# Optimization experiments

Hardware: AMD Instinct MI355X
Metric: run time of the kernel (lower is better)

The kernel has to match this reference:

```python
import jax, jax.numpy as jnp
from jax import lax
import numpy as np

B, H, W, D_MODEL = 2, 64, 64, 192
D_INNER, D_STATE, DT_RANK = 384, 16, 12
L = H * W
LN_EPS = 1e-5


def setup_inputs() -> dict:
    ks = jax.random.split(jax.random.key(0), 12)
    rng = np.random.default_rng(0)
    perm = rng.permutation(L).astype(np.int32)

    def p(i, shape, scale=0.02):
        return jax.random.normal(ks[i], shape, dtype=jnp.float32) * scale

    return {
        "x": jax.random.normal(ks[0], (B, H, W, D_MODEL), dtype=jnp.float32),
        "condition": jax.random.normal(ks[1], (B, H, W, D_MODEL), dtype=jnp.float32),
        "W_in": p(2, (2 * D_INNER, D_MODEL)),
        "W_con": p(3, (D_INNER, D_MODEL)),
        "conv_w": p(4, (D_INNER, 1, 3, 3)),
        "conv_b": jnp.zeros((D_INNER,), jnp.float32),
        "con_conv_w": p(5, (D_INNER, 1, 3, 3)),
        "con_conv_b": jnp.zeros((D_INNER,), jnp.float32),
        "x_proj_w": p(6, (DT_RANK + 2 * D_STATE, D_INNER)),
        "dt_proj_w": p(7, (D_INNER, DT_RANK)),
        "dt_proj_b": p(8, (D_INNER,), 0.1),
        "A_logs": jnp.tile(jnp.log(jnp.arange(1, D_STATE + 1, dtype=jnp.float32))[None, :], (D_INNER, 1)),
        "Ds": jnp.ones((D_INNER,), jnp.float32),
        "ln_w": jnp.ones((D_INNER,), jnp.float32),
        "ln_b": jnp.zeros((D_INNER,), jnp.float32),
        "W_out": p(9, (D_MODEL, D_INNER)),
        "scan_path": jnp.asarray(perm),
        "rev_scan_path": jnp.asarray(np.argsort(perm).astype(np.int32)),
    }


def _dwconv(x, w, b):
    # depthwise 3x3 conv, SAME padding; x: [B, C, H, W], w: [C, 1, 3, 3]
    y = lax.conv_general_dilated(x, w, (1, 1), "SAME",
                                 dimension_numbers=("NCHW", "OIHW", "NCHW"),
                                 feature_group_count=x.shape[1])
    return y + b[None, :, None, None]


def _selective_scan(u, delta, A, Bs, Cs, D):
    # u, delta: [B, D, L]; A: [D, N]; Bs, Cs: [B, N, L]; D: [D]
    dA = jnp.exp(jnp.einsum("bdl,dn->lbdn", delta, A))          # [L, B, D, N]
    dBu = jnp.einsum("bdl,bnl,bdl->lbdn", delta, Bs, u)          # [L, B, D, N]
    Ct = jnp.transpose(Cs, (2, 0, 1))                             # [L, B, N]
    h0 = jnp.zeros(dA.shape[1:], dA.dtype)

    def step(h, inp):
        a, b, c = inp
        h = a * h + b
        return h, jnp.einsum("bdn,bn->bd", h, c)

    _, ys = lax.scan(step, h0, (dA, dBu, Ct))                     # ys: [L, B, D]
    y = jnp.transpose(ys, (1, 2, 0))                              # [B, D, L]
    return y + u * D[None, :, None]


def _forward(x, condition, W_in, W_con, conv_w, conv_b, con_conv_w, con_conv_b,
             x_proj_w, dt_proj_w, dt_proj_b, A_logs, Ds, ln_w, ln_b, W_out,
             scan_path, rev_scan_path):
    b, h, w, _ = x.shape
    l = h * w
    xz = x @ W_in.T                                               # [B, H, W, 2*Din]
    xa, z = jnp.split(xz, 2, axis=-1)
    z = jax.nn.silu(z)
    c = condition @ W_con.T
    xa = jax.nn.silu(_dwconv(jnp.transpose(xa, (0, 3, 1, 2)), conv_w, conv_b))
    c = jax.nn.silu(_dwconv(jnp.transpose(c, (0, 3, 1, 2)), con_conv_w, con_conv_b))
    d = xa.shape[1]
    xs = xa.reshape(b, d, l)[:, :, scan_path]                     # forward_permutation, K=1
    cs = c.reshape(b, d, l)[:, :, scan_path]
    x_dbl = jnp.einsum("bdl,cd->bcl", xs + cs, x_proj_w)          # [B, R+2N, L]
    r, n = dt_proj_w.shape[1], A_logs.shape[1]
    dts = jnp.einsum("brl,dr->bdl", x_dbl[:, :r], dt_proj_w)
    Bs = x_dbl[:, r:r + n]
    Cs = x_dbl[:, r + n:]
    A = -jnp.exp(A_logs)
    delta = jax.nn.softplus(dts + dt_proj_b[None, :, None])       # delta_softplus=True
    y = _selective_scan(xs, delta, A, Bs, Cs, Ds)                 # [B, D, L]
    y = y[:, :, rev_scan_path]                                    # backward_permutation
    y = jnp.transpose(y, (0, 2, 1))                               # [B, L, D]
    mu = jnp.mean(y, axis=-1, keepdims=True)
    var = jnp.var(y, axis=-1, keepdims=True)
    y = (y - mu) * lax.rsqrt(var + LN_EPS) * ln_w + ln_b          # out_norm
    y = y.reshape(b, h, w, d) * z
    return y @ W_out.T                                            # out_proj (no bias)


def reference(x, condition, W_in, W_con, conv_w, conv_b, con_conv_w, con_conv_b,
              x_proj_w, dt_proj_w, dt_proj_b, A_logs, Ds, ln_w, ln_b, W_out,
              scan_path, rev_scan_path):
    return _forward(x, condition, W_in, W_con, conv_w, conv_b, con_conv_w,
                    con_conv_b, x_proj_w, dt_proj_w, dt_proj_b, A_logs, Ds,
                    ln_w, ln_b, W_out, scan_path, rev_scan_path)
```

## Files before the change

kernel.cpp:

```cpp
#include <hip/hip_runtime.h>
#include <math.h>

#define BB 2
#define HH 64
#define WW 64
#define DM 192
#define DI 384
#define NS 16
#define DTR 12
#define LL 4096
#define ROWS (BB*LL)
#define NCHUNK 128
#define LCHUNK 32
#define NCOMB 448
#define CSTRIDE ((size_t)BB * DI * 8)

typedef __attribute__((ext_vector_type(8))) short bf16x8;
typedef __attribute__((ext_vector_type(4))) float f32x4;

__device__ __forceinline__ float silu_f(float v) {
    return v / (1.0f + __expf(-v));
}

__device__ __forceinline__ unsigned short f2bf(float f) {
    union { float f; unsigned int u; } c; c.f = f;
    unsigned int u = c.u;
    u += 0x7fffu + ((u >> 16) & 1u);
    return (unsigned short)(u >> 16);
}
__device__ __forceinline__ float bf2f(unsigned short h) {
    union { unsigned int u; float f; } c; c.u = ((unsigned int)h) << 16;
    return c.f;
}

__device__ __forceinline__ bf16x8 f2bf8(float4 a, float4 b) {
    bf16x8 r;
    r[0] = (short)f2bf(a.x); r[1] = (short)f2bf(a.y);
    r[2] = (short)f2bf(a.z); r[3] = (short)f2bf(a.w);
    r[4] = (short)f2bf(b.x); r[5] = (short)f2bf(b.y);
    r[6] = (short)f2bf(b.z); r[7] = (short)f2bf(b.w);
    return r;
}

__global__ __launch_bounds__(256) void prep_weights(
    const float* __restrict__ w_in, const float* __restrict__ w_con,
    const float* __restrict__ w_out,
    const float* __restrict__ x_proj_w, const float* __restrict__ dt_w,
    unsigned short* __restrict__ w_in_bf, unsigned short* __restrict__ w_con_bf,
    unsigned short* __restrict__ w_out_bf, unsigned short* __restrict__ wc)
{
    int idx = blockIdx.x * 256 + threadIdx.x;
    if (idx < 73728) {
        const float4* src; ushort4* dst; int off;
        if (idx < 36864)      { src = (const float4*)w_in;  dst = (ushort4*)w_in_bf;  off = idx; }
        else if (idx < 55296) { src = (const float4*)w_con; dst = (ushort4*)w_con_bf; off = idx - 36864; }
        else                  { src = (const float4*)w_out; dst = (ushort4*)w_out_bf; off = idx - 55296; }
        float4 v = src[off];
        ushort4 o;
        o.x = f2bf(v.x); o.y = f2bf(v.y); o.z = f2bf(v.z); o.w = f2bf(v.w);
        dst[off] = o;
    } else {
        int e = idx - 73728;
        if (e >= NCOMB * DI) return;
        int row = e / DI, k = e - row * DI;
        float v = 0.f;
        if (row < 384) {
            const float* dw = dt_w + row * DTR;
            #pragma unroll
            for (int r = 0; r < DTR; ++r) v += dw[r] * x_proj_w[r * DI + k];
        } else if (row < 416) {
            v = x_proj_w[(12 + (row - 384)) * DI + k];
        }
        wc[e] = f2bf(v);
    }
}

__global__ __launch_bounds__(256) void gemm_bf16(
    const unsigned short* __restrict__ A, const unsigned short* __restrict__ W,
    const float* __restrict__ bias,
    float* __restrict__ out0, void* __restrict__ out1,
    unsigned short* __restrict__ du_lo,
    int M, int N, int K, int mode)
{
    __shared__ __align__(16) unsigned short sA[64 * 40];
    __shared__ __align__(16) unsigned short sB[64 * 40];
    const int bm = blockIdx.x * 64;
    const int bn = blockIdx.y * 64;
    const int tid  = threadIdx.x;
    const int wave = tid >> 6;
    const int lane = tid & 63;
    const int quad = lane >> 4;
    const int l16  = lane & 15;
    const int lrow = tid >> 2;
    const int lkof = (tid & 3) * 8;

    f32x4 acc[4];
    #pragma unroll
    for (int t = 0; t < 4; ++t) acc[t] = (f32x4)(0.f);

    const int arow = (wave * 16 + l16) * 40 + quad * 8;

    for (int k0 = 0; k0 < K; k0 += 32) {
        *(bf16x8*)&sA[lrow * 40 + lkof] =
            *(const bf16x8*)&A[(size_t)(bm + lrow) * K + k0 + lkof];
        *(bf16x8*)&sB[lrow * 40 + lkof] =
            *(const bf16x8*)&W[(size_t)(bn + lrow) * K + k0 + lkof];
        __syncthreads();
        bf16x8 a = *(bf16x8*)&sA[arow];
        #pragma unroll
        for (int t = 0; t < 4; ++t) {
            bf16x8 b = *(bf16x8*)&sB[(t * 16 + l16) * 40 + quad * 8];
            acc[t] = __builtin_amdgcn_mfma_f32_16x16x32_bf16(a, b, acc[t], 0, 0, 0);
        }
        __syncthreads();
    }

    #pragma unroll
    for (int t = 0; t < 4; ++t) {
        int col = bn + t * 16 + l16;
        #pragma unroll
        for (int r = 0; r < 4; ++r) {
            int row = bm + wave * 16 + quad * 4 + r;
            float v = acc[t][r];
            if (mode == 1) {
                out0[(size_t)row * N + col] = v;
            } else {
                if (col < 384) {
                    float a = v + bias[col];
                    float sp = (a > 20.f) ? a : log1pf(__expf(a));
                    du_lo[((size_t)row * 384 + col) * 2] = f2bf(sp);
                } else if (col < 416) {
                    int idx = col - 384;
                    int pos = (idx < 16) ? ((idx & 7) * 4 + (idx >> 3))
                                         : (((idx - 16) & 7) * 4 + 2 + ((idx - 16) >> 3));
                    ((float*)out1)[(size_t)row * 32 + pos] = v;
                }
            }
        }
    }
}

__global__ __launch_bounds__(256) void gemm_dual(
    const float* __restrict__ x, const float* __restrict__ cond,
    const unsigned short* __restrict__ w_in_bf,
    const unsigned short* __restrict__ w_con_bf,
    unsigned short* __restrict__ xa_bf, unsigned short* __restrict__ z_bf,
    unsigned short* __restrict__ c_bf)
{
    const int zz = blockIdx.z;
    if (zz == 1 && blockIdx.y >= 6) return;
    const float* A = zz ? cond : x;
    const unsigned short* W = zz ? w_con_bf : w_in_bf;

    __shared__ __align__(16) unsigned short sA[64 * 40];
    __shared__ __align__(16) unsigned short sB[64 * 40];
    const int bm = blockIdx.x * 64;
    const int bn = blockIdx.y * 64;
    const int tid  = threadIdx.x;
    const int wave = tid >> 6;
    const int lane = tid & 63;
    const int quad = lane >> 4;
    const int l16  = lane & 15;
    const int lrow = tid >> 2;
    const int lkof = (tid & 3) * 8;

    f32x4 acc[4];
    #pragma unroll
    for (int t = 0; t < 4; ++t) acc[t] = (f32x4)(0.f);

    const int arow = (wave * 16 + l16) * 40 + quad * 8;

    for (int k0 = 0; k0 < DM; k0 += 32) {
        const float* ap = &A[(size_t)(bm + lrow) * DM + k0 + lkof];
        float4 a0 = *(const float4*)ap;
        float4 a1 = *(const float4*)(ap + 4);
        *(bf16x8*)&sA[lrow * 40 + lkof] = f2bf8(a0, a1);
        *(bf16x8*)&sB[lrow * 40 + lkof] =
            *(const bf16x8*)&W[(size_t)(bn + lrow) * DM + k0 + lkof];
        __syncthreads();
        bf16x8 a = *(bf16x8*)&sA[arow];
        #pragma unroll
        for (int t = 0; t < 4; ++t) {
            bf16x8 b = *(bf16x8*)&sB[(t * 16 + l16) * 40 + quad * 8];
            acc[t] = __builtin_amdgcn_mfma_f32_16x16x32_bf16(a, b, acc[t], 0, 0, 0);
        }
        __syncthreads();
    }

    #pragma unroll
    for (int t = 0; t < 4; ++t) {
        int col = bn + t * 16 + l16;
        #pragma unroll
        for (int r = 0; r < 4; ++r) {
            int row = bm + wave * 16 + quad * 4 + r;
            float v = acc[t][r];
            if (zz == 0) {
                if (col < 384) xa_bf[(size_t)row * 384 + col] = f2bf(v);
                else           z_bf[(size_t)row * 384 + (col - 384)] = f2bf(silu_f(v));
            } else {
                c_bf[(size_t)row * 384 + col] = f2bf(v);
            }
        }
    }
}

__global__ __launch_bounds__(256) void dwconv2_scatter(
    const unsigned short* __restrict__ xin, const unsigned short* __restrict__ cin,
    const float* __restrict__ wx, const float* __restrict__ bx,
    const float* __restrict__ wc, const float* __restrict__ bc,
    const int* __restrict__ rev_scan_path,
    unsigned short* __restrict__ du_hi,
    unsigned short* __restrict__ s_bf)
{
    const int tile = blockIdx.x;
    const int c0   = blockIdx.y * 32;
    const int b    = blockIdx.z;
    const int h0 = (tile >> 3) * 8, w0 = (tile & 7) * 8;
    __shared__ float smx[10 * 10 * 32];
    __shared__ float smc[10 * 10 * 32];
    __shared__ int   jtile[64];

    for (int idx = threadIdx.x; idx < 3200; idx += 256) {
        int pix = idx >> 5, ch = idx & 31;
        int py = pix / 10, px = pix - py * 10;
        int gh = h0 + py - 1, gw = w0 + px - 1;
        float vx = 0.f, vc = 0.f;
        if (gh >= 0 && gh < 64 && gw >= 0 && gw < 64) {
            size_t g = ((size_t)(b * LL + gh * 64 + gw)) * DI + c0 + ch;
            vx = bf2f(xin[g]); vc = bf2f(cin[g]);
        }
        smx[idx] = vx; smc[idx] = vc;
    }
    if (threadIdx.x < 64) {
        int l = (h0 + (threadIdx.x >> 3)) * 64 + (w0 + (threadIdx.x & 7));
        jtile[threadIdx.x] = rev_scan_path[l];
    }
    __syncthreads();

    const int ch = threadIdx.x & 31;
    const int pq = threadIdx.x >> 5;
    float wrx[9], wrc[9];
    #pragma unroll
    for (int k = 0; k < 9; ++k) {
        wrx[k] = wx[(c0 + ch) * 9 + k];
        wrc[k] = wc[(c0 + ch) * 9 + k];
    }
    const float bvx = bx[c0 + ch];
    const float bvc = bc[c0 + ch];

    #pragma unroll
    for (int i = 0; i < 8; ++i) {
        int p  = pq * 8 + i;
        int ph = p >> 3, pw = p & 7;
        float ax = bvx, ac = bvc;
        #pragma unroll
        for (int ki = 0; ki < 3; ++ki)
            #pragma unroll
            for (int kj = 0; kj < 3; ++kj) {
                int si = ((ph + ki) * 10 + (pw + kj)) * 32 + ch;
                ax += wrx[ki * 3 + kj] * smx[si];
                ac += wrc[ki * 3 + kj] * smc[si];
            }
        float xv = silu_f(ax);
        float sv = xv + silu_f(ac);
        size_t o = ((size_t)(b * LL + jtile[p])) * DI + c0 + ch;
        du_hi[o * 2 + 1] = f2bf(xv);
        s_bf[o]          = f2bf(sv);
    }
}

__global__ __launch_bounds__(256) void scan_chunkA(
    const unsigned int* __restrict__ du, const float* __restrict__ btct,
    const float* __restrict__ A_logs,
    float* __restrict__ chunkA, float* __restrict__ chunkB)
{
    const int c = blockIdx.x;
    const int g = blockIdx.y;
    const int b = blockIdx.z;
    const int t = threadIdx.x;
    const int grp = t >> 3, p = t & 7;
    const int d = g * 32 + grp;
    const float Av0 = -__expf(A_logs[d * NS + p]);
    const float Av1 = -__expf(A_logs[d * NS + p + 8]);
    const int j0 = c * LCHUNK;

    const unsigned int* dul = du + ((size_t)b * LL + j0) * DI + d;
    const float2*       bl  = (const float2*)btct + ((size_t)b * LL + j0) * 16 + p * 2;

    float h0 = 0.f, h1 = 0.f, Sd = 0.f;
    unsigned int duv[4]; float2 bv[4];
    #pragma unroll
    for (int q = 0; q < 4; ++q) {
        duv[q] = dul[(size_t)q * DI]; bv[q] = bl[(size_t)q * 16];
    }
    for (int j = 0; j < LCHUNK; j += 4) {
        unsigned int ndu[4]; float2 nb[4];
        if (j + 4 < LCHUNK) {
            #pragma unroll
            for (int q = 0; q < 4; ++q) {
                int jj = j + 4 + q;
                ndu[q] = dul[(size_t)jj * DI]; nb[q] = bl[(size_t)jj * 16];
            }
        }
        #pragma unroll
        for (int q = 0; q < 4; ++q) {
            float dv = bf2f((unsigned short)(duv[q] & 0xffff));
            float uv = bf2f((unsigned short)(duv[q] >> 16));
            float e0 = __expf(dv * Av0);
            float e1 = __expf(dv * Av1);
            float duu = dv * uv;
            h0 = e0 * h0 + bv[q].x * duu;
            h1 = e1 * h1 + bv[q].y * duu;
            Sd += dv;
        }
        #pragma unroll
        for (int q = 0; q < 4; ++q) { duv[q]=ndu[q]; bv[q]=nb[q]; }
    }
    size_t idx = (size_t)c * CSTRIDE + ((size_t)b * DI + d) * 8 + p;
    ((float2*)chunkA)[idx] = make_float2(__expf(Sd * Av0), __expf(Sd * Av1));
    ((float2*)chunkB)[idx] = make_float2(h0, h1);
}

__global__ __launch_bounds__(256) void scan_chunkC(
    const unsigned int* __restrict__ du, const float* __restrict__ btct,
    const float* __restrict__ A_logs, const float* __restrict__ Ds,
    const float* __restrict__ chunkA, const float* __restrict__ chunkB,
    unsigned short* __restrict__ yt)
{
    const int c = blockIdx.x;
    const int g = blockIdx.y;
    const int b = blockIdx.z;
    const int t = threadIdx.x;
    const int grp = t >> 3, p = t & 7;
    const int d = g * 32 + grp;
    const float Av0 = -__expf(A_logs[d * NS + p]);
    const float Av1 = -__expf(A_logs[d * NS + p + 8]);
    const float Dv = Ds[d];
    const int j0 = c * LCHUNK;

    const unsigned int* dul = du + ((size_t)b * LL + j0) * DI + d;
    const float4*       bcl = (const float4*)btct + ((size_t)b * LL + j0) * 8 + p;
    unsigned short* yl = yt + ((size_t)b * LL + j0) * DI + d;

    const size_t off = ((size_t)b * DI + d) * 8 + p;
    const float2* A2 = (const float2*)chunkA;
    const float2* B2 = (const float2*)chunkB;
    float h0 = 0.f, h1 = 0.f, P0 = 1.f, P1 = 1.f;
    for (int i = c - 1; i >= 0; --i) {
        size_t ix = (size_t)i * CSTRIDE + off;
        float2 a = A2[ix], bv = B2[ix];
        h0 += P0 * bv.x;  h1 += P1 * bv.y;
        P0 *= a.x;        P1 *= a.y;
        if (fmaxf(fabsf(P0), fabsf(P1)) < 1e-30f) break;
    }

    unsigned int duv[4]; float4 bc[4];
    #pragma unroll
    for (int q = 0; q < 4; ++q) {
        duv[q] = dul[(size_t)q * DI]; bc[q] = bcl[(size_t)q * 8];
    }
    for (int j = 0; j < LCHUNK; j += 4) {
        unsigned int ndu[4]; float4 nbc[4];
        if (j + 4 < LCHUNK) {
            #pragma unroll
            for (int q = 0; q < 4; ++q) {
                int jj = j + 4 + q;
                ndu[q] = dul[(size_t)jj * DI]; nbc[q] = bcl[(size_t)jj * 8];
            }
        }
        #pragma unroll
        for (int q = 0; q < 4; ++q) {
            float dv = bf2f((unsigned short)(duv[q] & 0xffff));
            float uv = bf2f((unsigned short)(duv[q] >> 16));
            float e0 = __expf(dv * Av0);
            float e1 = __expf(dv * Av1);
            float duu = dv * uv;
            h0 = e0 * h0 + bc[q].x * duu;
            h1 = e1 * h1 + bc[q].y * duu;
            float acc = h0 * bc[q].z + h1 * bc[q].w;
            acc += __shfl_xor(acc, 4, 8);
            acc += __shfl_xor(acc, 2, 8);
            acc += __shfl_xor(acc, 1, 8);
            if (p == 0) yl[(size_t)(j + q) * DI] = f2bf(acc + uv * Dv);
        }
        #pragma unroll
        for (int q = 0; q < 4; ++q) { duv[q]=ndu[q]; bc[q]=nbc[q]; }
    }
}

__global__ __launch_bounds__(128) void ln_mul(
    const unsigned short* __restrict__ yt, const unsigned short* __restrict__ z,
    const int* __restrict__ scan_path,
    const float* __restrict__ ln_w, const float* __restrict__ ln_b,
    unsigned short* __restrict__ yn)
{
    const int j = blockIdx.x;
    const int b = blockIdx.y;
    const int l = scan_path[j];
    const int t = threadIdx.x;
    const unsigned short* row = yt + ((size_t)(b * LL + j)) * DI;
    float v0 = bf2f(row[t]), v1 = bf2f(row[t + 128]), v2 = bf2f(row[t + 256]);
    float s  = v0 + v1 + v2;
    float s2 = v0*v0 + v1*v1 + v2*v2;
    #pragma unroll
    for (int off = 32; off > 0; off >>= 1) {
        s  += __shfl_down(s, off);
        s2 += __shfl_down(s2, off);
    }
    __shared__ float red[4];
    if ((t & 63) == 0) { red[(t >> 6) * 2] = s; red[(t >> 6) * 2 + 1] = s2; }
    __syncthreads();
    float S  = red[0] + red[2];
    float S2 = red[1] + red[3];
    float mu  = S * (1.0f / DI);
    float var = S2 * (1.0f / DI) - mu * mu;
    float inv = rsqrtf(var + 1e-5f);

    const unsigned short* zr = z + ((size_t)(b * LL + l)) * DI;
    unsigned short* o = yn + ((size_t)(b * LL + l)) * DI;
    o[t]       = f2bf(((v0 - mu) * inv * ln_w[t]       + ln_b[t])       * bf2f(zr[t]));
    o[t + 128] = f2bf(((v1 - mu) * inv * ln_w[t + 128] + ln_b[t + 128]) * bf2f(zr[t + 128]));
    o[t + 256] = f2bf(((v2 - mu) * inv * ln_w[t + 256] + ln_b[t + 256]) * bf2f(zr[t + 256]));
}

extern "C" void kernel_launch(void* const* d_in, const int* in_sizes, int n_in,
                              void* d_out, int out_size, void* d_ws, size_t ws_size,
                              hipStream_t stream) {
    const float* x          = (const float*)d_in[0];
    const float* cond       = (const float*)d_in[1];
    const float* W_in       = (const float*)d_in[2];
    const float* W_con      = (const float*)d_in[3];
    const float* conv_w     = (const float*)d_in[4];
    const float* conv_b     = (const float*)d_in[5];
    const float* con_conv_w = (const float*)d_in[6];
    const float* con_conv_b = (const float*)d_in[7];
    const float* x_proj_w   = (const float*)d_in[8];
    const float* dt_proj_w  = (const float*)d_in[9];
    const float* dt_proj_b  = (const float*)d_in[10];
    const float* A_logs     = (const float*)d_in[11];
    const float* Ds         = (const float*)d_in[12];
    const float* ln_w       = (const float*)d_in[13];
    const float* ln_b       = (const float*)d_in[14];
    const float* W_out      = (const float*)d_in[15];
    const int*   scan_path  = (const int*)d_in[16];
    const int*   rev_path   = (const int*)d_in[17];

    float* ws = (float*)d_ws;
    const size_t S  = (size_t)BB * LL * DI;
    const size_t SC = (size_t)NCHUNK * BB * DI * NS;
    float* ytslab  = ws + 0 * S;
    float* zslab   = ws + 1 * S;
    float* ynslab  = ws + 2 * S;
    float* duslab  = ws + 3 * S;
    float* btct    = ws + 4 * S;
    float* chunkA  = btct + (size_t)BB * LL * 32;
    float* chunkB  = chunkA + SC;
    float* bfpool  = chunkB + SC;

    unsigned short* yt_bf    = (unsigned short*)ytslab;
    unsigned short* z_bf     = (unsigned short*)zslab;
    unsigned short* yn_bf    = (unsigned short*)ynslab;
    unsigned int*   du       = (unsigned int*)duslab;
    unsigned short* s_bf     = (unsigned short*)bfpool;
    unsigned short* xa_bf    = s_bf + (size_t)ROWS * DI;
    unsigned short* c_bf     = xa_bf + (size_t)ROWS * DI;
    unsigned short* w_in_bf  = c_bf + (size_t)ROWS * DI;
    unsigned short* w_con_bf = w_in_bf + 768 * DM;
    unsigned short* w_out_bf = w_con_bf + 384 * DM;
    unsigned short* wcomb_bf = w_out_bf + 192 * DI;

    prep_weights<<<(73728 + NCOMB * DI + 255) / 256, 256, 0, stream>>>(
        W_in, W_con, W_out, x_proj_w, dt_proj_w,
        w_in_bf, w_con_bf, w_out_bf, wcomb_bf);

    gemm_dual<<<dim3(ROWS / 64, 12, 2), 256, 0, stream>>>(
        x, cond, w_in_bf, w_con_bf, xa_bf, z_bf, c_bf);
    dwconv2_scatter<<<dim3(64, 12, BB), 256, 0, stream>>>(
        xa_bf, c_bf, conv_w, conv_b, con_conv_w, con_conv_b,
        rev_path, (unsigned short*)du, s_bf);
    gemm_bf16<<<dim3(ROWS / 64, NCOMB / 64), 256, 0, stream>>>(
        s_bf, wcomb_bf, dt_proj_b, nullptr, (void*)btct,
        (unsigned short*)du, ROWS, NCOMB, DI, 2);
    scan_chunkA<<<dim3(NCHUNK, DI / 32, BB), 256, 0, stream>>>(
        du, btct, A_logs, chunkA, chunkB);
    scan_chunkC<<<dim3(NCHUNK, DI / 32, BB), 256, 0, stream>>>(
        du, btct, A_logs, Ds, chunkA, chunkB, yt_bf);
    ln_mul<<<dim3(LL, BB), 128, 0, stream>>>(yt_bf, z_bf, scan_path, ln_w, ln_b, yn_bf);
    gemm_bf16<<<dim3(ROWS / 64, 192 / 64), 256, 0, stream>>>(
        yn_bf, w_out_bf, nullptr, (float*)d_out, nullptr, nullptr, ROWS, DM, DI, 1);
}
```

Baseline: 203.5 us.

## Use direct global-to-LDS loads and 128-row tiles in projection GEMMs

The GEMM kernels now stage tiles with global_load_lds 16-byte async copies into unpadded LDS instead of going through registers. The input and combined-projection GEMMs compute 128x64 tiles per block, with two accumulator row fragments per wave, so each B tile is reused twice. The fp32 x and condition inputs are converted to bf16 in the prep kernel, so the input GEMM can use the direct LDS path. Risks are LDS bank conflicts from dropping the padding, fewer blocks per GEMM, and an extra pass and buffer for the input conversion.

```diff
diff --git a/kernel.cpp b/kernel.cpp
--- a/kernel.cpp
+++ b/kernel.cpp
@@ -18,6 +18,13 @@
 typedef __attribute__((ext_vector_type(8))) short bf16x8;
 typedef __attribute__((ext_vector_type(4))) float f32x4;
 
+typedef __attribute__((address_space(3))) void        as3_void;
+typedef __attribute__((address_space(1))) const void  as1_cvoid;
+
+__device__ __forceinline__ void gl_lds16(const unsigned short* g, unsigned short* l) {
+    __builtin_amdgcn_global_load_lds((as1_cvoid*)g, (as3_void*)l, 16, 0, 0);
+}
+
 __device__ __forceinline__ float silu_f(float v) {
     return v / (1.0f + __expf(-v));
 }
@@ -33,21 +40,14 @@
     return c.f;
 }
 
-__device__ __forceinline__ bf16x8 f2bf8(float4 a, float4 b) {
-    bf16x8 r;
-    r[0] = (short)f2bf(a.x); r[1] = (short)f2bf(a.y);
-    r[2] = (short)f2bf(a.z); r[3] = (short)f2bf(a.w);
-    r[4] = (short)f2bf(b.x); r[5] = (short)f2bf(b.y);
-    r[6] = (short)f2bf(b.z); r[7] = (short)f2bf(b.w);
-    return r;
-}
-
 __global__ __launch_bounds__(256) void prep_weights(
+    const float* __restrict__ x, const float* __restrict__ cond,
     const float* __restrict__ w_in, const float* __restrict__ w_con,
     const float* __restrict__ w_out,
     const float* __restrict__ x_proj_w, const float* __restrict__ dt_w,
     unsigned short* __restrict__ w_in_bf, unsigned short* __restrict__ w_con_bf,
-    unsigned short* __restrict__ w_out_bf, unsigned short* __restrict__ wc)
+    unsigned short* __restrict__ w_out_bf, unsigned short* __restrict__ wc,
+    unsigned short* __restrict__ x_bfo, unsigned short* __restrict__ c_bfo)
 {
     int idx = blockIdx.x * 256 + threadIdx.x;
     if (idx < 73728) {
@@ -59,9 +59,8 @@
         ushort4 o;
         o.x = f2bf(v.x); o.y = f2bf(v.y); o.z = f2bf(v.z); o.w = f2bf(v.w);
         dst[off] = o;
-    } else {
+    } else if (idx < 73728 + NCOMB * DI) {
         int e = idx - 73728;
-        if (e >= NCOMB * DI) return;
         int row = e / DI, k = e - row * DI;
         float v = 0.f;
         if (row < 384) {
@@ -72,59 +71,152 @@
             v = x_proj_w[(12 + (row - 384)) * DI + k];
         }
         wc[e] = f2bf(v);
-    }
-}
-
-__global__ __launch_bounds__(256) void gemm_bf16(
-    const unsigned short* __restrict__ A, const unsigned short* __restrict__ W,
-    const float* __restrict__ bias,
-    float* __restrict__ out0, void* __restrict__ out1,
-    unsigned short* __restrict__ du_lo,
-    int M, int N, int K, int mode)
-{
-    __shared__ __align__(16) unsigned short sA[64 * 40];
-    __shared__ __align__(16) unsigned short sB[64 * 40];
-    const int bm = blockIdx.x * 64;
+    } else if (idx < 73728 + NCOMB * DI + 786432) {
+        int e = idx - (73728 + NCOMB * DI);
+        const float4* src; ushort4* dst; int off;
+        if (e < 393216) { src = (const float4*)x;    dst = (ushort4*)x_bfo; off = e; }
+        else            { src = (const float4*)cond; dst = (ushort4*)c_bfo; off = e - 393216; }
+        float4 v = src[off];
+        ushort4 o;
+        o.x = f2bf(v.x); o.y = f2bf(v.y); o.z = f2bf(v.z); o.w = f2bf(v.w);
+        dst[off] = o;
+    }
+}
+
+__global__ __launch_bounds__(256) void gemm_in(
+    const unsigned short* __restrict__ x_bf, const unsigned short* __restrict__ cin_bf,
+    const unsigned short* __restrict__ w_in_bf,
+    const unsigned short* __restrict__ w_con_bf,
+    unsigned short* __restrict__ xa_bf, unsigned short* __restrict__ z_bf,
+    unsigned short* __restrict__ c_bf)
+{
+    const int zz = blockIdx.z;
+    if (zz == 1 && blockIdx.y >= 6) return;
+    const unsigned short* A = zz ? cin_bf : x_bf;
+    const unsigned short* W = zz ? w_con_bf : w_in_bf;
+
+    __shared__ __align__(16) unsigned short sA[128 * 32];
+    __shared__ __align__(16) unsigned short sB[64 * 32];
+    const int bm = blockIdx.x * 128;
     const int bn = blockIdx.y * 64;
     const int tid  = threadIdx.x;
     const int wave = tid >> 6;
     const int lane = tid & 63;
     const int quad = lane >> 4;
     const int l16  = lane & 15;
-    const int lrow = tid >> 2;
-    const int lkof = (tid & 3) * 8;
-
-    f32x4 acc[4];
-    #pragma unroll
-    for (int t = 0; t < 4; ++t) acc[t] = (f32x4)(0.f);
-
-    const int arow = (wave * 16 + l16) * 40 + quad * 8;
-
-    for (int k0 = 0; k0 < K; k0 += 32) {
-        *(bf16x8*)&sA[lrow * 40 + lkof] =
-            *(const bf16x8*)&A[(size_t)(bm + lrow) * K + k0 + lkof];
-        *(bf16x8*)&sB[lrow * 40 + lkof] =
-            *(const bf16x8*)&W[(size_t)(bn + lrow) * K + k0 + lkof];
+    const int srow = tid >> 2;
+    const int scol = (tid & 3) * 8;
+
+    f32x4 acc[2][4];
+    #pragma unroll
+    for (int rf = 0; rf < 2; ++rf)
+        #pragma unroll
+        for (int t = 0; t < 4; ++t) acc[rf][t] = (f32x4)(0.f);
+
+    const unsigned short* gA0 = &A[(size_t)(bm + srow) * DM + scol];
+    const unsigned short* gA1 = gA0 + (size_t)64 * DM;
+    const unsigned short* gB  = &W[(size_t)(bn + srow) * DM + scol];
+    unsigned short* lA0 = &sA[wave * 512];
+    unsigned short* lA1 = &sA[2048 + wave * 512];
+    unsigned short* lB  = &sB[wave * 512];
+
+    const int ar0 = (wave * 32 + l16) * 32 + quad * 8;
+    const int ar1 = ar0 + 16 * 32;
+
+    for (int k0 = 0; k0 < DM; k0 += 32) {
+        gl_lds16(gA0 + k0, lA0);
+        gl_lds16(gA1 + k0, lA1);
+        gl_lds16(gB  + k0, lB);
         __syncthreads();
-        bf16x8 a = *(bf16x8*)&sA[arow];
+        bf16x8 a0 = *(bf16x8*)&sA[ar0];
+        bf16x8 a1 = *(bf16x8*)&sA[ar1];
         #pragma unroll
         for (int t = 0; t < 4; ++t) {
-            bf16x8 b = *(bf16x8*)&sB[(t * 16 + l16) * 40 + quad * 8];
-            acc[t] = __builtin_amdgcn_mfma_f32_16x16x32_bf16(a, b, acc[t], 0, 0, 0);
+            bf16x8 b = *(bf16x8*)&sB[(t * 16 + l16) * 32 + quad * 8];
+            acc[0][t] = __builtin_amdgcn_mfma_f32_16x16x32_bf16(a0, b, acc[0][t], 0, 0, 0);
+            acc[1][t] = __builtin_amdgcn_mfma_f32_16x16x32_bf16(a1, b, acc[1][t], 0, 0, 0);
         }
         __syncthreads();
     }
 
     #pragma unroll
-    for (int t = 0; t < 4; ++t) {
-        int col = bn + t * 16 + l16;
-        #pragma unroll
-        for (int r = 0; r < 4; ++r) {
-            int row = bm + wave * 16 + quad * 4 + r;
-            float v = acc[t][r];
-            if (mode == 1) {
-                out0[(size_t)row * N + col] = v;
-            } else {
+    for (int rf = 0; rf < 2; ++rf) {
+        #pragma unroll
+        for (int t = 0; t < 4; ++t) {
+            int col = bn + t * 16 + l16;
+            #pragma unroll
+            for (int r = 0; r < 4; ++r) {
+                int row = bm + wave * 32 + rf * 16 + quad * 4 + r;
+                float v = acc[rf][t][r];
+                if (zz == 0) {
+                    if (col < 384) xa_bf[(size_t)row * 384 + col] = f2bf(v);
+                    else           z_bf[(size_t)row * 384 + (col - 384)] = f2bf(silu_f(v));
+                } else {
+                    c_bf[(size_t)row * 384 + col] = f2bf(v);
+                }
+            }
+        }
+    }
+}
+
+__global__ __launch_bounds__(256) void gemm_comb(
+    const unsigned short* __restrict__ A, const unsigned short* __restrict__ W,
+    const float* __restrict__ bias, float* __restrict__ btct,
+    unsigned short* __restrict__ du_lo)
+{
+    __shared__ __align__(16) unsigned short sA[128 * 32];
+    __shared__ __align__(16) unsigned short sB[64 * 32];
+    const int bm = blockIdx.x * 128;
+    const int bn = blockIdx.y * 64;
+    const int tid  = threadIdx.x;
+    const int wave = tid >> 6;
+    const int lane = tid & 63;
+    const int quad = lane >> 4;
+    const int l16  = lane & 15;
+    const int srow = tid >> 2;
+    const int scol = (tid & 3) * 8;
+
+    f32x4 acc[2][4];
+    #pragma unroll
+    for (int rf = 0; rf < 2; ++rf)
+        #pragma unroll
+        for (int t = 0; t < 4; ++t) acc[rf][t] = (f32x4)(0.f);
+
+    const unsigned short* gA0 = &A[(size_t)(bm + srow) * DI + scol];
+    const unsigned short* gA1 = gA0 + (size_t)64 * DI;
+    const unsigned short* gB  = &W[(size_t)(bn + srow) * DI + scol];
+    unsigned short* lA0 = &sA[wave * 512];
+    unsigned short* lA1 = &sA[2048 + wave * 512];
+    unsigned short* lB  = &sB[wave * 512];
+
+    const int ar0 = (wave * 32 + l16) * 32 + quad * 8;
+    const int ar1 = ar0 + 16 * 32;
+
+    for (int k0 = 0; k0 < DI; k0 += 32) {
+        gl_lds16(gA0 + k0, lA0);
+        gl_lds16(gA1 + k0, lA1);
+        gl_lds16(gB  + k0, lB);
+        __syncthreads();
+        bf16x8 a0 = *(bf16x8*)&sA[ar0];
+        bf16x8 a1 = *(bf16x8*)&sA[ar1];
+        #pragma unroll
+        for (int t = 0; t < 4; ++t) {
+            bf16x8 b = *(bf16x8*)&sB[(t * 16 + l16) * 32 + quad * 8];
+            acc[0][t] = __builtin_amdgcn_mfma_f32_16x16x32_bf16(a0, b, acc[0][t], 0, 0, 0);
+            acc[1][t] = __builtin_amdgcn_mfma_f32_16x16x32_bf16(a1, b, acc[1][t], 0, 0, 0);
+        }
+        __syncthreads();
+    }
+
+    #pragma unroll
+    for (int rf = 0; rf < 2; ++rf) {
+        #pragma unroll
+        for (int t = 0; t < 4; ++t) {
+            int col = bn + t * 16 + l16;
+            #pragma unroll
+            for (int r = 0; r < 4; ++r) {
+                int row = bm + wave * 32 + rf * 16 + quad * 4 + r;
+                float v = acc[rf][t][r];
                 if (col < 384) {
                     float a = v + bias[col];
                     float sp = (a > 20.f) ? a : log1pf(__expf(a));
@@ -133,27 +225,19 @@
                     int idx = col - 384;
                     int pos = (idx < 16) ? ((idx & 7) * 4 + (idx >> 3))
                                          : (((idx - 16) & 7) * 4 + 2 + ((idx - 16) >> 3));
-                    ((float*)out1)[(size_t)row * 32 + pos] = v;
+                    btct[(size_t)row * 32 + pos] = v;
                 }
             }
         }
     }
 }
 
-__global__ __launch_bounds__(256) void gemm_dual(
-    const float* __restrict__ x, const float* __restrict__ cond,
-    const unsigned short* __restrict__ w_in_bf,
-    const unsigned short* __restrict__ w_con_bf,
-    unsigned short* __restrict__ xa_bf, unsigned short* __restrict__ z_bf,
-    unsigned short* __restrict__ c_bf)
-{
-    const int zz = blockIdx.z;
-    if (zz == 1 && blockIdx.y >= 6) return;
-    const float* A = zz ? cond : x;
-    const unsigned short* W = zz ? w_con_bf : w_in_bf;
-
-    __shared__ __align__(16) unsigned short sA[64 * 40];
-    __shared__ __align__(16) unsigned short sB[64 * 40];
+__global__ __launch_bounds__(256) void gemm_outk(
+    const unsigned short* __restrict__ A, const unsigned short* __restrict__ W,
+    float* __restrict__ out)
+{
+    __shared__ __align__(16) unsigned short sA[64 * 32];
+    __shared__ __align__(16) unsigned short sB[64 * 32];
     const int bm = blockIdx.x * 64;
     const int bn = blockIdx.y * 64;
     const int tid  = threadIdx.x;
@@ -161,27 +245,28 @@
     const int lane = tid & 63;
     const int quad = lane >> 4;
     const int l16  = lane & 15;
-    const int lrow = tid >> 2;
-    const int lkof = (tid & 3) * 8;
+    const int srow = tid >> 2;
+    const int scol = (tid & 3) * 8;
 
     f32x4 acc[4];
     #pragma unroll
     for (int t = 0; t < 4; ++t) acc[t] = (f32x4)(0.f);
 
-    const int arow = (wave * 16 + l16) * 40 + quad * 8;
-
-    for (int k0 = 0; k0 < DM; k0 += 32) {
-        const float* ap = &A[(size_t)(bm + lrow) * DM + k0 + lkof];
-        float4 a0 = *(const float4*)ap;
-        float4 a1 = *(const float4*)(ap + 4);
-        *(bf16x8*)&sA[lrow * 40 + lkof] = f2bf8(a0, a1);
-        *(bf16x8*)&sB[lrow * 40 + lkof] =
-            *(const bf16x8*)&W[(size_t)(bn + lrow) * DM + k0 + lkof];
+    const unsigned short* gA = &A[(size_t)(bm + srow) * DI + scol];
+    const unsigned short* gB = &W[(size_t)(bn + srow) * DI + scol];
+    unsigned short* lA = &sA[wave * 512];
+    unsigned short* lB = &sB[wave * 512];
+
+    const int arow = (wave * 16 + l16) * 32 + quad * 8;
+
+    for (int k0 = 0; k0 < DI; k0 += 32) {
+        gl_lds16(gA + k0, lA);
+        gl_lds16(gB + k0, lB);
         __syncthreads();
         bf16x8 a = *(bf16x8*)&sA[arow];
         #pragma unroll
         for (int t = 0; t < 4; ++t) {
-            bf16x8 b = *(bf16x8*)&sB[(t * 16 + l16) * 40 + quad * 8];
+            bf16x8 b = *(bf16x8*)&sB[(t * 16 + l16) * 32 + quad * 8];
             acc[t] = __builtin_amdgcn_mfma_f32_16x16x32_bf16(a, b, acc[t], 0, 0, 0);
         }
         __syncthreads();
@@ -193,13 +278,7 @@
         #pragma unroll
         for (int r = 0; r < 4; ++r) {
             int row = bm + wave * 16 + quad * 4 + r;
-            float v = acc[t][r];
-            if (zz == 0) {
-                if (col < 384) xa_bf[(size_t)row * 384 + col] = f2bf(v);
-                else           z_bf[(size_t)row * 384 + (col - 384)] = f2bf(silu_f(v));
-            } else {
-                c_bf[(size_t)row * 384 + col] = f2bf(v);
-            }
+            out[(size_t)row * DM + col] = acc[t][r];
         }
     }
 }
@@ -468,24 +547,24 @@
     unsigned short* w_con_bf = w_in_bf + 768 * DM;
     unsigned short* w_out_bf = w_con_bf + 384 * DM;
     unsigned short* wcomb_bf = w_out_bf + 192 * DI;
-
-    prep_weights<<<(73728 + NCOMB * DI + 255) / 256, 256, 0, stream>>>(
-        W_in, W_con, W_out, x_proj_w, dt_proj_w,
-        w_in_bf, w_con_bf, w_out_bf, wcomb_bf);
-
-    gemm_dual<<<dim3(ROWS / 64, 12, 2), 256, 0, stream>>>(
-        x, cond, w_in_bf, w_con_bf, xa_bf, z_bf, c_bf);
+    unsigned short* x_bf2    = wcomb_bf + (size_t)NCOMB * DI;
+    unsigned short* cin_bf2  = x_bf2 + (size_t)ROWS * DM;
+
+    prep_weights<<<4032, 256, 0, stream>>>(
+        x, cond, W_in, W_con, W_out, x_proj_w, dt_proj_w,
+        w_in_bf, w_con_bf, w_out_bf, wcomb_bf, x_bf2, cin_bf2);
+
+    gemm_in<<<dim3(ROWS / 128, 12, 2), 256, 0, stream>>>(
+        x_bf2, cin_bf2, w_in_bf, w_con_bf, xa_bf, z_bf, c_bf);
     dwconv2_scatter<<<dim3(64, 12, BB), 256, 0, stream>>>(
         xa_bf, c_bf, conv_w, conv_b, con_conv_w, con_conv_b,
         rev_path, (unsigned short*)du, s_bf);
-    gemm_bf16<<<dim3(ROWS / 64, NCOMB / 64), 256, 0, stream>>>(
-        s_bf, wcomb_bf, dt_proj_b, nullptr, (void*)btct,
-        (unsigned short*)du, ROWS, NCOMB, DI, 2);
+    gemm_comb<<<dim3(ROWS / 128, NCOMB / 64), 256, 0, stream>>>(
+        s_bf, wcomb_bf, dt_proj_b, btct, (unsigned short*)du);
     scan_chunkA<<<dim3(NCHUNK, DI / 32, BB), 256, 0, stream>>>(
         du, btct, A_logs, chunkA, chunkB);
     scan_chunkC<<<dim3(NCHUNK, DI / 32, BB), 256, 0, stream>>>(
         du, btct, A_logs, Ds, chunkA, chunkB, yt_bf);
     ln_mul<<<dim3(LL, BB), 128, 0, stream>>>(yt_bf, z_bf, scan_path, ln_w, ln_b, yn_bf);
-    gemm_bf16<<<dim3(ROWS / 64, 192 / 64), 256, 0, stream>>>(
-        yn_bf, w_out_bf, nullptr, (float*)d_out, nullptr, nullptr, ROWS, DM, DI, 1);
-}
+    gemm_outk<<<dim3(ROWS / 64, DM / 64), 256, 0, stream>>>(yn_bf, w_out_bf, (float*)d_out);
+}
```

Result: no change. 206.6 us (+1.5%).
